# Kernel tuning notes

Hardware: AMD Instinct MI355X
Metric: run time of the kernel (lower is better)

## Reference

```python
import jax, jax.numpy as jnp
import numpy as np

T, N = 64, 1048576  # bitstream length, number of parallel unary channels


def setup_inputs() -> dict:
    key = jax.random.key(0)
    kbits = jax.random.fold_in(key, 1)
    # unary bitstream: each bit is 0 or 1 (Bernoulli(0.5)); stored as float,
    # matching bstype=torch.float output / int8-on-{0,1} internal math exactly.
    bits = (jax.random.uniform(kbits, (T, N)) < 0.5).astype(jnp.float32)
    trace0 = jnp.zeros((N,), jnp.float32)  # JKFF state, torch inits zeros(1)
    return {"input": bits, "trace0": trace0}


def reference(input, trace0):
    # UnarySqrt with emit=False, mode='unipolar', jk_trace=True.
    # Per torch forward (python precedence: `1 - trace & input` == (1-trace)&input):
    #   output = ((1 - trace) & input) + trace
    #   trace' = JKFF(J=output, K=1)  ->  Q' = J & ~Q = output & (1 - trace)
    # On {0,1} bits, AND == multiply; the add is disjoint so stays exact.
    def step(trace, x):
        out = (1.0 - trace) * x + trace
        trace_next = out * (1.0 - trace)
        return trace_next, out

    _, outs = jax.lax.scan(step, trace0, input)  # outs: [T, N]
    return outs
```

## Files before the change

kernel.cpp:

```cpp
#include <hip/hip_runtime.h>
#include <stdint.h>


typedef float v4f __attribute__((ext_vector_type(4)));

__global__ __launch_bounds__(1024) void UnarySqrt_kernel(
    const v4f* __restrict__ in,
    const v4f* __restrict__ trace0,
    v4f* __restrict__ out,
    int stride)
{
    const int idx = blockIdx.x * blockDim.x + threadIdx.x;
    if (idx >= stride) return;

    v4f tr = trace0[idx];

    for (int c = 0; c < 8; ++c) {
        v4f buf[8];
        #pragma unroll
        for (int j = 0; j < 8; ++j) {
            buf[j] = in[(size_t)(c * 8 + j) * (size_t)stride + (size_t)idx];
        }
        asm volatile("" : "+v"(buf[0]), "+v"(buf[1]), "+v"(buf[2]), "+v"(buf[3]),
                          "+v"(buf[4]), "+v"(buf[5]), "+v"(buf[6]), "+v"(buf[7]));
        #pragma unroll
        for (int j = 0; j < 8; ++j) {
            v4f p = buf[j] * (1.0f - tr);
            v4f o = tr + p;
            __builtin_nontemporal_store(
                o, &out[(size_t)(c * 8 + j) * (size_t)stride + (size_t)idx]);
            tr = p;
        }
    }
}

__global__ __launch_bounds__(256) void UnarySqrt_generic(
    const v4f* __restrict__ in, const v4f* __restrict__ trace0,
    v4f* __restrict__ out, int stride, int T)
{
    int idx = blockIdx.x * blockDim.x + threadIdx.x;
    if (idx >= stride) return;
    v4f tr = trace0[idx];
    for (int t = 0; t < T; ++t) {
        v4f x = in[(size_t)t * stride + idx];
        v4f p = x * (1.0f - tr);
        out[(size_t)t * stride + idx] = tr + p;
        tr = p;
    }
}

extern "C" void kernel_launch(void* const* d_in, const int* in_sizes, int n_in,
                              void* d_out, int out_size, void* d_ws, size_t ws_size,
                              hipStream_t stream) {
    const float* bits   = (const float*)d_in[0];
    const float* trace0 = (const float*)d_in[1];

    int N = in_sizes[1];
    int T = in_sizes[0] / N;
    int stride = N / 4;

    if (T == 64 && (stride % 1024) == 0) {
        int grid = stride / 1024;
        UnarySqrt_kernel<<<grid, 1024, 0, stream>>>(
            (const v4f*)bits, (const v4f*)trace0, (v4f*)d_out, stride);
    } else {
        int block = 256;
        int grid = (stride + block - 1) / block;
        UnarySqrt_generic<<<grid, block, 0, stream>>>(
            (const v4f*)bits, (const v4f*)trace0, (v4f*)d_out, stride, T);
    }
}
```

Baseline: 448.9 us.

## Pace blocks through time chunks with a grid-wide soft barrier

Adds a global atomic counter per time chunk so all blocks advance through the 8-row chunks roughly in lockstep. A bounded spin-wait with sleep stops blocks from drifting apart, which is meant to keep DRAM access streams localized to a few row ranges. It also switches the loads to nontemporal and the stores to normal, and adds an extra init kernel launch. The cost is barrier stalls and atomics; the spin limit avoids deadlock if not all blocks are resident at once.

After: 557.1 us. 1.24x slower.

```diff
diff --git a/kernel.cpp b/kernel.cpp
--- a/kernel.cpp
+++ b/kernel.cpp
@@ -4,32 +4,55 @@
 
 typedef float v4f __attribute__((ext_vector_type(4)));
 
+#define RPC 8
+#define NCHK 8
+
+__global__ void pace_init(int* cnt) {
+    if (threadIdx.x < 16) cnt[threadIdx.x] = 0;
+}
+
 __global__ __launch_bounds__(1024) void UnarySqrt_kernel(
     const v4f* __restrict__ in,
     const v4f* __restrict__ trace0,
     v4f* __restrict__ out,
-    int stride)
+    int stride,
+    int* __restrict__ cnt,
+    int nblocks)
 {
     const int idx = blockIdx.x * blockDim.x + threadIdx.x;
     if (idx >= stride) return;
 
     v4f tr = trace0[idx];
 
-    for (int c = 0; c < 8; ++c) {
-        v4f buf[8];
+    for (int c = 0; c < NCHK; ++c) {
+        v4f buf[RPC];
         #pragma unroll
-        for (int j = 0; j < 8; ++j) {
-            buf[j] = in[(size_t)(c * 8 + j) * (size_t)stride + (size_t)idx];
+        for (int j = 0; j < RPC; ++j) {
+            buf[j] = __builtin_nontemporal_load(
+                &in[(size_t)(c * RPC + j) * (size_t)stride + (size_t)idx]);
         }
         asm volatile("" : "+v"(buf[0]), "+v"(buf[1]), "+v"(buf[2]), "+v"(buf[3]),
                           "+v"(buf[4]), "+v"(buf[5]), "+v"(buf[6]), "+v"(buf[7]));
         #pragma unroll
-        for (int j = 0; j < 8; ++j) {
+        for (int j = 0; j < RPC; ++j) {
             v4f p = buf[j] * (1.0f - tr);
             v4f o = tr + p;
-            __builtin_nontemporal_store(
-                o, &out[(size_t)(c * 8 + j) * (size_t)stride + (size_t)idx]);
+            out[(size_t)(c * RPC + j) * (size_t)stride + (size_t)idx] = o;
             tr = p;
+        }
+        if (c + 1 < NCHK) {
+            __syncthreads();
+            if (threadIdx.x == 0) {
+                __hip_atomic_fetch_add(&cnt[c], 1, __ATOMIC_RELAXED,
+                                       __HIP_MEMORY_SCOPE_AGENT);
+                int lim = 150;
+                while (__hip_atomic_load(&cnt[c], __ATOMIC_RELAXED,
+                                         __HIP_MEMORY_SCOPE_AGENT) < nblocks
+                       && --lim) {
+                    __builtin_amdgcn_s_sleep(2);
+                }
+            }
+            __syncthreads();
         }
     }
 }
@@ -61,8 +84,10 @@
 
     if (T == 64 && (stride % 1024) == 0) {
         int grid = stride / 1024;
+        int* cnt = (int*)d_ws;
+        pace_init<<<1, 64, 0, stream>>>(cnt);
         UnarySqrt_kernel<<<grid, 1024, 0, stream>>>(
-            (const v4f*)bits, (const v4f*)trace0, (v4f*)d_out, stride);
+            (const v4f*)bits, (const v4f*)trace0, (v4f*)d_out, stride, cnt, grid);
     } else {
         int block = 256;
         int grid = (stride + block - 1) / block;
```
